# Kernel optimization log

Measured on AMD Instinct MI355X. Metric: run time of the kernel, lower is better.

Reference implementation:

```python
import jax, jax.numpy as jnp
import numpy as np

B, HH, WW, DV, DC = 4, 128, 128, 768, 128
INNER = 2 * DV          # inner_ratio * values_dim = 1536
NH = 8                  # num_heads
DH = INNER // NH        # 192
SPACING = 4
COORDS_WEIGHT = 1.0     # attention_coords_weight
EPS = 1e-6


def _anchor_idx(h, w, s, shifted=False):
    rows = np.arange(0, h, s)
    cols = np.arange(0, w, s)
    if not shifted:
        rows = rows + ((h - 1) % s) // 2
        cols = cols + ((w - 1) % s) // 2
    return rows, cols


def _rms(x, w):
    return x * jax.lax.rsqrt(jnp.mean(x * x, axis=-1, keepdims=True) + EPS) * w


def _heads(x):  # (b, n, h*d) -> (b, h, n, d)
    b, n, _ = x.shape
    return x.reshape(b, n, NH, DH).transpose(0, 2, 1, 3)


def setup_inputs() -> dict:
    key = jax.random.key(0)
    ks = jax.random.split(key, 12)
    inp = {
        "values0": jax.random.normal(ks[0], (B, HH, WW, DV), jnp.float32),
        "coords0": jax.random.normal(ks[1], (B, HH, WW, DC), jnp.float32),
        "values1": jax.random.normal(ks[2], (B, HH, WW, DV), jnp.float32),
        "coords1": jax.random.normal(ks[3], (B, HH, WW, DC), jnp.float32),
        # values_to_qkv: Linear(DV, 3*INNER, bias=False), stored as (in, out)
        "w_qkv": jax.random.normal(ks[4], (DV, 3 * INNER), jnp.float32) * (DV ** -0.5),
        "qnorm_w": jnp.ones((INNER,), jnp.float32),
        "knorm_w": jnp.ones((INNER,), jnp.float32),
        # coords_to_qk: Linear(DC, 2*INNER, bias=False) + RMSNorm(2*INNER)
        "w_coords": jax.random.normal(ks[5], (DC, 2 * INNER), jnp.float32) * (DC ** -0.5),
        "coords_norm_w": jnp.ones((2 * INNER,), jnp.float32),
        "rel_pos_weight": jax.random.normal(ks[6], (1,), jnp.float32),
        # output_proj: Linear(INNER, DV)
        "out_w": jax.random.normal(ks[7], (INNER, DV), jnp.float32) * (INNER ** -0.5),
        "out_b": jnp.zeros((DV,), jnp.float32),
    }
    return inp


def reference(values0, coords0, values1, coords1, w_qkv, qnorm_w, knorm_w,
              w_coords, coords_norm_w, rel_pos_weight, out_w, out_b):
    rows, cols = _anchor_idx(HH, WW, SPACING)
    na = len(rows) * len(cols)  # anchors per source (1024)

    def gather(x):  # (B, HH, WW, D) -> (B, na, D)
        return x[:, rows[:, None], cols].reshape(B, na, -1)

    av = jnp.concatenate([gather(values0), gather(values1)], axis=1)  # (B, 2na, DV)
    ac = jnp.concatenate([gather(coords0), gather(coords1)], axis=1)  # (B, 2na, DC)

    qv, kv, vv = jnp.split(av @ w_qkv, 3, axis=-1)
    qv = _rms(qv, qnorm_w)
    kv = _rms(kv, knorm_w)
    qc, kc = jnp.split(_rms(ac @ w_coords, coords_norm_w), 2, axis=-1)

    qv, kv, vv, qc, kc = map(_heads, (qv, kv, vv, qc, kc))  # (B, NH, N, DH)

    scale = DH ** -0.5
    dots = jnp.einsum('bhqd,bhkd->bhqk', qv, kv) * scale
    rel = jnp.einsum('bhqd,bhkd->bhqk', qc, kc) * scale
    dots = dots + (rel_pos_weight[0] * COORDS_WEIGHT) * rel
    attn = jax.nn.softmax(dots, axis=-1)

    out = jnp.einsum('bhqk,bhkd->bhqd', attn, vv)          # (B, NH, N, DH)
    out = out.transpose(0, 2, 1, 3).reshape(B, 2 * na, INNER)
    out = out @ out_w + out_b                               # (B, 2na, DV)

    a0 = out[:, :na].reshape(B, len(rows), len(cols), DV)
    a1 = out[:, na:].reshape(B, len(rows), len(cols), DV)

    o0 = values0.at[:, rows[:, None], cols, :].add(a0)
    o1 = values1.at[:, rows[:, None], cols, :].add(a1)
    return jnp.stack([o0, o1])  # (2, B, HH, WW, DV)
```

## Files before the change

### kernel.cpp

```cpp
#include <hip/hip_runtime.h>

typedef unsigned short u16;
typedef unsigned int u32;
typedef float f32x4 __attribute__((ext_vector_type(4)));
typedef short bfx8 __attribute__((ext_vector_type(8)));
typedef u16 u16x8 __attribute__((ext_vector_type(8)));
typedef u16 u16x4 __attribute__((ext_vector_type(4)));

#define MFMA_BF16(a,b,c) __builtin_amdgcn_mfma_f32_16x16x32_bf16((a),(b),(c),0,0,0)
#define GL16(src, dst) __builtin_amdgcn_global_load_lds( \
    (const __attribute__((address_space(1))) u32*)(src), \
    (__attribute__((address_space(3))) u32*)(dst), 16, 0, 0)

__device__ __forceinline__ u16 f2bf(float f) {
  unsigned u = __float_as_uint(f);
  u += 0x7fffu + ((u >> 16) & 1u);
  return (u16)(u >> 16);
}
__device__ __forceinline__ float bf2f(u16 h) {
  return __uint_as_float((unsigned)h << 16);
}

#define SCALE_ATTN 0.07216878364870323f

__global__ __launch_bounds__(256) void wtrans_kernel(
    const float* __restrict__ in, u16* __restrict__ out, int K, int N)
{
  __shared__ float tile[32][33];
  int n0 = blockIdx.x * 32, k0 = blockIdx.y * 32;
  int tx = threadIdx.x, ty = threadIdx.y;
#pragma unroll
  for (int j = 0; j < 32; j += 8)
    tile[ty + j][tx] = in[(size_t)(k0 + ty + j) * N + n0 + tx];
  __syncthreads();
#pragma unroll
  for (int j = 0; j < 32; j += 8)
    out[(size_t)(n0 + ty + j) * K + k0 + tx] = f2bf(tile[tx][ty + j]);
}

__global__ __launch_bounds__(256) void gather_kernel(
    const float* __restrict__ v0, const float* __restrict__ c0,
    const float* __restrict__ v1, const float* __restrict__ c1,
    u16* __restrict__ av, u16* __restrict__ ac)
{
  int t = blockIdx.x;
  int b = t >> 11, n = t & 2047, s = n >> 10, a = n & 1023, rr = a >> 5, cc = a & 31;
  size_t pix = ((size_t)b * 128 + (1 + 4 * rr)) * 128 + (1 + 4 * cc);
  const float4* vs = (const float4*)((s ? v1 : v0) + pix * 768);
  const float4* cs = (const float4*)((s ? c1 : c0) + pix * 128);
  int tid = threadIdx.x;
  if (tid < 192) {
    float4 f = vs[tid];
    u16x4 o = { f2bf(f.x), f2bf(f.y), f2bf(f.z), f2bf(f.w) };
    *(u16x4*)(av + (size_t)t * 768 + tid * 4) = o;
  }
  if (tid < 32) {
    float4 f = cs[tid];
    u16x4 o = { f2bf(f.x), f2bf(f.y), f2bf(f.z), f2bf(f.w) };
    *(u16x4*)(ac + (size_t)t * 128 + tid * 4) = o;
  }
}

template<int EPILOG>
__global__ __launch_bounds__(256) void gemm128(
    const u16* __restrict__ A, const u16* __restrict__ Bt,
    int K, int lda, int ldb,
    u16* __restrict__ qp, u16* __restrict__ kp, u16* __restrict__ vT,
    float* __restrict__ outAdd, const float* __restrict__ bias)
{
  __shared__ u16 As[128 * 32];
  __shared__ u16 Bs[128 * 32];
  const int tid = threadIdx.x;
  const int wid = tid >> 6, lane = tid & 63;
  const int g = lane >> 4, q15 = lane & 15;
  const int wm = wid >> 1, wn = wid & 1;
  const int m0 = blockIdx.y * 128, n0 = blockIdx.x * 128;

  const u16* ga = A + (size_t)(m0 + (tid >> 2)) * lda + (tid & 3) * 8;
  const u16* gb = Bt + (size_t)(n0 + (tid >> 2)) * ldb + (tid & 3) * 8;
  u16* lA0 = &As[tid * 8]; u16* lA1 = &As[2048 + tid * 8];
  u16* lB0 = &Bs[tid * 8]; u16* lB1 = &Bs[2048 + tid * 8];
  const size_t a64 = (size_t)64 * lda, b64 = (size_t)64 * ldb;

  const f32x4 zero = {0.f, 0.f, 0.f, 0.f};
  f32x4 acc[4][4];
#pragma unroll
  for (int i = 0; i < 4; i++)
#pragma unroll
    for (int j = 0; j < 4; j++) acc[i][j] = zero;

  for (int kk = 0; kk < K; kk += 32) {
    GL16(ga + kk, lA0);
    GL16(ga + kk + a64, lA1);
    GL16(gb + kk, lB0);
    GL16(gb + kk + b64, lB1);
    __syncthreads();
    bfx8 af[4], bf[4];
#pragma unroll
    for (int mt = 0; mt < 4; mt++)
      af[mt] = *(const bfx8*)&As[(wm * 64 + mt * 16 + q15) * 32 + g * 8];
#pragma unroll
    for (int nt = 0; nt < 4; nt++)
      bf[nt] = *(const bfx8*)&Bs[(wn * 64 + nt * 16 + q15) * 32 + g * 8];
#pragma unroll
    for (int mt = 0; mt < 4; mt++)
#pragma unroll
      for (int nt = 0; nt < 4; nt++)
        acc[mt][nt] = MFMA_BF16(af[mt], bf[nt], acc[mt][nt]);
    __syncthreads();
  }

#pragma unroll
  for (int mt = 0; mt < 4; mt++) {
#pragma unroll
    for (int nt = 0; nt < 4; nt++) {
      const int tt = m0 + wm * 64 + mt * 16 + g * 4;
      const int c = n0 + wn * 64 + nt * 16 + q15;
      f32x4 v = acc[mt][nt];
      if (EPILOG == 0) {
        int isK = c >= 1536;
        int ck = isK ? c - 1536 : c;
        int hh = ck / 192, dd = ck - hh * 192;
#pragma unroll
        for (int j = 0; j < 4; j++) {
          int t = tt + j, b = t >> 11, n = t & 2047;
          size_t ro = ((size_t)(b * 8 + hh) * 2048 + n) * 384;
          u16 val = f2bf(v[j]);
          if (!isK) qp[ro + 192 + dd] = val;
          else      kp[ro + (size_t)((((24 + (dd >> 3)) ^ (n & 7)) << 3) + (dd & 7))] = val;
        }
      } else if (EPILOG == 1) {
        float bb = bias[c];
#pragma unroll
        for (int j = 0; j < 4; j++) {
          int t = tt + j, b = t >> 11, n = t & 2047;
          int s = n >> 10, a = n & 1023, rr = a >> 5, cc2 = a & 31;
          size_t orow = (size_t)(s * 4 + b) * 16384 + (size_t)(1 + 4 * rr) * 128 + (1 + 4 * cc2);
          outAdd[orow * 768 + c] += v[j] + bb;
        }
      } else {
        if (c < 1536) {
          int hh = c / 192, dd = c - hh * 192;
#pragma unroll
          for (int j = 0; j < 4; j++) {
            int t = tt + j, b = t >> 11, n = t & 2047;
            size_t ro = ((size_t)(b * 8 + hh) * 2048 + n) * 384;
            qp[ro + dd] = f2bf(v[j]);
          }
        } else if (c < 3072) {
          int ck = c - 1536;
          int hh = ck / 192, dd = ck - hh * 192;
          int chunk = dd >> 3, e = dd & 7;
#pragma unroll
          for (int j = 0; j < 4; j++) {
            int t = tt + j, b = t >> 11, n = t & 2047;
            size_t ro = ((size_t)(b * 8 + hh) * 2048 + n) * 384;
            kp[ro + (size_t)(((chunk ^ (n & 7)) << 3) + e)] = f2bf(v[j]);
          }
        } else {
          int cv = c - 3072;
          int hh = cv / 192, dv = cv - hh * 192;
          int t0 = tt, b = t0 >> 11, n = t0 & 2047;
          u16x4 o = { f2bf(v[0]), f2bf(v[1]), f2bf(v[2]), f2bf(v[3]) };
          *(u16x4*)(vT + ((size_t)(b * 8 + hh) * 192 + dv) * 2048 + n) = o;
        }
      }
    }
  }
}

__global__ __launch_bounds__(256) void rms_all_kernel(
    u16* __restrict__ qpack, u16* __restrict__ kpack,
    const float* __restrict__ qnw, const float* __restrict__ knw,
    const float* __restrict__ cnw, const float* __restrict__ relw)
{
  __shared__ float red[3][4];
  int t = blockIdx.x, tid = threadIdx.x;
  int b = t >> 11, n = t & 2047;
  float sqv = 0.f, skv = 0.f, sc = 0.f;
  u16x8 uqv, ukv, uqc, ukc;
  size_t ro = 0;
  int c = 0;
  if (tid < 192) {
    int h = tid / 24; c = tid % 24;
    ro = ((size_t)(b * 8 + h) * 2048 + n) * 384;
    uqv = *(const u16x8*)(qpack + ro + c * 8);
    ukv = *(const u16x8*)(kpack + ro + ((c ^ (n & 7)) * 8));
    uqc = *(const u16x8*)(qpack + ro + 192 + c * 8);
    ukc = *(const u16x8*)(kpack + ro + (((24 + c) ^ (n & 7)) * 8));
#pragma unroll
    for (int e = 0; e < 8; e++) {
      float a = bf2f(uqv[e]); sqv += a * a;
      float d = bf2f(ukv[e]); skv += d * d;
      float x = bf2f(uqc[e]); sc += x * x;
      float y = bf2f(ukc[e]); sc += y * y;
    }
  }
#pragma unroll
  for (int o = 32; o >= 1; o >>= 1) {
    sqv += __shfl_xor(sqv, o); skv += __shfl_xor(skv, o); sc += __shfl_xor(sc, o);
  }
  int wv = tid >> 6;
  if ((tid & 63) == 0) { red[0][wv] = sqv; red[1][wv] = skv; red[2][wv] = sc; }
  __syncthreads();
  sqv = red[0][0] + red[0][1] + red[0][2] + red[0][3];
  skv = red[1][0] + red[1][1] + red[1][2] + red[1][3];
  sc  = red[2][0] + red[2][1] + red[2][2] + red[2][3];
  float fqv = rsqrtf(sqv * (1.f / 1536.f) + 1e-6f) * SCALE_ATTN;
  float fkv = rsqrtf(skv * (1.f / 1536.f) + 1e-6f);
  float fc  = rsqrtf(sc * (1.f / 3072.f) + 1e-6f);
  float fqc = fc * SCALE_ATTN * relw[0];
  if (tid < 192) {
    u16x8 o0, o1, o2, o3;
#pragma unroll
    for (int e = 0; e < 8; e++) {
      int col = tid * 8 + e;
      o0[e] = f2bf(bf2f(uqv[e]) * fqv * qnw[col]);
      o1[e] = f2bf(bf2f(ukv[e]) * fkv * knw[col]);
      o2[e] = f2bf(bf2f(uqc[e]) * fqc * cnw[col]);
      o3[e] = f2bf(bf2f(ukc[e]) * fc  * cnw[1536 + col]);
    }
    *(u16x8*)(qpack + ro + c * 8) = o0;
    *(u16x8*)(kpack + ro + ((c ^ (n & 7)) * 8)) = o1;
    *(u16x8*)(qpack + ro + 192 + c * 8) = o2;
    *(u16x8*)(kpack + ro + (((24 + c) ^ (n & 7)) * 8)) = o3;
  }
}

__global__ __launch_bounds__(256, 2) void attn_kernel(
    const u16* __restrict__ qpack, const u16* __restrict__ kpack,
    const u16* __restrict__ vT, u16* __restrict__ attnO)
{
  __shared__ u16 Ks[2][32 * 384];
  __shared__ u16 Vs[2][192 * 32];

  const int tid = threadIdx.x;
  const int wid = tid >> 6, lane = tid & 63;
  const int g = lane >> 4, q15 = lane & 15;
  const int bid = blockIdx.x;
  const int bh = (bid & 7) * 4 + ((bid >> 3) >> 4);
  const int q0 = ((bid >> 3) & 15) * 128 + wid * 32;
  const int b = bh >> 3, h = bh & 7;
  const int sw = q15 & 7;
  const int vsw = g ^ (q15 & 3);
  const bool hi = g >= 2;
  const int srcA = q15 + ((g & 1) << 5);

  bfx8 qf[2][12];
  {
    const u16* qb = qpack + ((size_t)bh * 2048 + q0 + q15) * 384 + g * 8;
#pragma unroll
    for (int s = 0; s < 2; s++)
#pragma unroll
      for (int c = 0; c < 12; c++)
        qf[s][c] = *(const bfx8*)(qb + s * 16 * 384 + c * 32);
  }

  const f32x4 zero = {0.f, 0.f, 0.f, 0.f};
  f32x4 acc[2][12];
#pragma unroll
  for (int s = 0; s < 2; s++)
#pragma unroll
    for (int i = 0; i < 12; i++) acc[s][i] = zero;
  float m0 = -3e30f, m1 = -3e30f, l0 = 0.f, l1 = 0.f;

  const char* kg = (const char*)(kpack + (size_t)bh * 2048 * 384);
  const char* vg = (const char*)(vT + (size_t)bh * 192 * 2048);

  auto stage = [&](int buf, int kb) {
    const char* ks = kg + (size_t)kb * 768;
#pragma unroll
    for (int j = 0; j < 6; j++) {
      int off = j * 4096 + tid * 16;
      GL16(ks + off, (char*)&Ks[buf][0] + off);
    }
    const char* vsrc = vg + (size_t)kb * 2;
#pragma unroll
    for (int j = 0; j < 3; j++) {
      int off = j * 4096 + tid * 16;
      int row = off >> 6;
      int cc = (tid & 3) ^ (row & 3);
      GL16(vsrc + (size_t)row * 4096 + cc * 16, (char*)&Vs[buf][0] + off);
    }
  };

  stage(0, 0);
  __syncthreads();

  int cur = 0;
  for (int t = 0; t < 64; t++) {
    if (t < 63) stage(cur ^ 1, (t + 1) * 32);

    f32x4 s00 = zero, s01 = zero, s10 = zero, s11 = zero;
    const u16* Kc = &Ks[cur][0];
#pragma unroll
    for (int c = 0; c < 12; c++) {
      int ch = ((((c << 2) + g) ^ sw) << 3);
      bfx8 k0 = *(const bfx8*)(Kc + q15 * 384 + ch);
      bfx8 k1 = *(const bfx8*)(Kc + (q15 + 16) * 384 + ch);
      s00 = MFMA_BF16(k0, qf[0][c], s00);
      s01 = MFMA_BF16(k0, qf[1][c], s01);
      s10 = MFMA_BF16(k1, qf[0][c], s10);
      s11 = MFMA_BF16(k1, qf[1][c], s11);
    }

    float bm0 = fmaxf(fmaxf(fmaxf(s00[0], s00[1]), fmaxf(s00[2], s00[3])),
                      fmaxf(fmaxf(s10[0], s10[1]), fmaxf(s10[2], s10[3])));
    float bm1 = fmaxf(fmaxf(fmaxf(s01[0], s01[1]), fmaxf(s01[2], s01[3])),
                      fmaxf(fmaxf(s11[0], s11[1]), fmaxf(s11[2], s11[3])));
    bm0 = fmaxf(bm0, __shfl_xor(bm0, 16)); bm0 = fmaxf(bm0, __shfl_xor(bm0, 32));
    bm1 = fmaxf(bm1, __shfl_xor(bm1, 16)); bm1 = fmaxf(bm1, __shfl_xor(bm1, 32));

    if (__any((bm0 > m0 + 8.f) | (bm1 > m1 + 8.f))) {
      float n0 = fmaxf(m0, bm0), n1 = fmaxf(m1, bm1);
      float c0 = __expf(m0 - n0), c1 = __expf(m1 - n1);
      l0 *= c0; l1 *= c1;
#pragma unroll
      for (int i = 0; i < 12; i++) {
#pragma unroll
        for (int j = 0; j < 4; j++) { acc[0][i][j] *= c0; acc[1][i][j] *= c1; }
      }
      m0 = n0; m1 = n1;
    }

    float p0[8], p1[8];
    float rs0 = 0.f, rs1 = 0.f;
#pragma unroll
    for (int j = 0; j < 4; j++) {
      p0[j]     = __expf(s00[j] - m0);
      p0[4 + j] = __expf(s10[j] - m0);
      p1[j]     = __expf(s01[j] - m1);
      p1[4 + j] = __expf(s11[j] - m1);
      rs0 += p0[j] + p0[4 + j];
      rs1 += p1[j] + p1[4 + j];
    }
    rs0 += __shfl_xor(rs0, 16); rs0 += __shfl_xor(rs0, 32);
    rs1 += __shfl_xor(rs1, 16); rs1 += __shfl_xor(rs1, 32);
    l0 += rs0; l1 += rs1;

    union { bfx8 v; u32 w[4]; } pt0, pt1;
    {
      u32 w0 = (u32)f2bf(p0[0]) | ((u32)f2bf(p0[1]) << 16);
      u32 w1 = (u32)f2bf(p0[2]) | ((u32)f2bf(p0[3]) << 16);
      u32 w2 = (u32)f2bf(p0[4]) | ((u32)f2bf(p0[5]) << 16);
      u32 w3 = (u32)f2bf(p0[6]) | ((u32)f2bf(p0[7]) << 16);
      u32 a0 = __shfl((int)w0, srcA),      b0 = __shfl((int)w2, srcA);
      u32 a1 = __shfl((int)w1, srcA),      b1 = __shfl((int)w3, srcA);
      u32 a2 = __shfl((int)w0, srcA + 16), b2 = __shfl((int)w2, srcA + 16);
      u32 a3 = __shfl((int)w1, srcA + 16), b3 = __shfl((int)w3, srcA + 16);
      pt0.w[0] = hi ? b0 : a0; pt0.w[1] = hi ? b1 : a1;
      pt0.w[2] = hi ? b2 : a2; pt0.w[3] = hi ? b3 : a3;
    }
    {
      u32 w0 = (u32)f2bf(p1[0]) | ((u32)f2bf(p1[1]) << 16);
      u32 w1 = (u32)f2bf(p1[2]) | ((u32)f2bf(p1[3]) << 16);
      u32 w2 = (u32)f2bf(p1[4]) | ((u32)f2bf(p1[5]) << 16);
      u32 w3 = (u32)f2bf(p1[6]) | ((u32)f2bf(p1[7]) << 16);
      u32 a0 = __shfl((int)w0, srcA),      b0 = __shfl((int)w2, srcA);
      u32 a1 = __shfl((int)w1, srcA),      b1 = __shfl((int)w3, srcA);
      u32 a2 = __shfl((int)w0, srcA + 16), b2 = __shfl((int)w2, srcA + 16);
      u32 a3 = __shfl((int)w1, srcA + 16), b3 = __shfl((int)w3, srcA + 16);
      pt1.w[0] = hi ? b0 : a0; pt1.w[1] = hi ? b1 : a1;
      pt1.w[2] = hi ? b2 : a2; pt1.w[3] = hi ? b3 : a3;
    }

    const u16* Vc = &Vs[cur][0];
#pragma unroll
    for (int dt = 0; dt < 12; dt++) {
      bfx8 vf = *(const bfx8*)(Vc + dt * 512 + q15 * 32 + vsw * 8);
      acc[0][dt] = MFMA_BF16(vf, pt0.v, acc[0][dt]);
      acc[1][dt] = MFMA_BF16(vf, pt1.v, acc[1][dt]);
    }

    asm volatile("s_waitcnt vmcnt(0)" ::: "memory");
    __syncthreads();
    cur ^= 1;
  }

  float li0 = 1.f / l0, li1 = 1.f / l1;
  u16* ob = attnO + ((size_t)(b * 2048 + q0 + q15)) * 1536 + h * 192;
#pragma unroll
  for (int dt = 0; dt < 12; dt++) {
    u16x4 o0, o1;
#pragma unroll
    for (int j = 0; j < 4; j++) {
      o0[j] = f2bf(acc[0][dt][j] * li0);
      o1[j] = f2bf(acc[1][dt][j] * li1);
    }
    *(u16x4*)(ob + dt * 16 + g * 4) = o0;
    *(u16x4*)(ob + (size_t)16 * 1536 + dt * 16 + g * 4) = o1;
  }
}

extern "C" void kernel_launch(void* const* d_in, const int* in_sizes, int n_in,
                              void* d_out, int out_size, void* d_ws, size_t ws_size,
                              hipStream_t stream)
{
  const float* values0 = (const float*)d_in[0];
  const float* coords0 = (const float*)d_in[1];
  const float* values1 = (const float*)d_in[2];
  const float* coords1 = (const float*)d_in[3];
  const float* w_qkv   = (const float*)d_in[4];
  const float* qnorm_w = (const float*)d_in[5];
  const float* knorm_w = (const float*)d_in[6];
  const float* w_coords= (const float*)d_in[7];
  const float* cnorm_w = (const float*)d_in[8];
  const float* relw    = (const float*)d_in[9];
  const float* out_w   = (const float*)d_in[10];
  const float* out_b   = (const float*)d_in[11];
  float* out = (float*)d_out;
  (void)in_sizes; (void)n_in; (void)out_size; (void)ws_size;

  char* ws = (char*)d_ws;
  u16* qpack   = (u16*)(ws);
  u16* kpack   = (u16*)(ws + 50331648ull);
  u16* vT      = (u16*)(ws + 100663296ull);
  u16* attnO   = (u16*)(ws + 125829120ull);
  u16* av      = (u16*)(ws + 150994944ull);
  u16* ac      = (u16*)(ws + 163577856ull);
  u16* wqkvT   = (u16*)(ws + 165675008ull);
  u16* wcoordT = (u16*)(ws + 172752896ull);
  u16* outwT   = (u16*)(ws + 173539328ull);

  const size_t HALF = 50331648ull;
  hipMemcpyAsync(out, values0, HALF * 4, hipMemcpyDeviceToDevice, stream);
  hipMemcpyAsync(out + HALF, values1, HALF * 4, hipMemcpyDeviceToDevice, stream);

  wtrans_kernel<<<dim3(144, 24), dim3(32, 8), 0, stream>>>(w_qkv, wqkvT, 768, 4608);
  wtrans_kernel<<<dim3(96, 4),   dim3(32, 8), 0, stream>>>(w_coords, wcoordT, 128, 3072);
  wtrans_kernel<<<dim3(24, 48),  dim3(32, 8), 0, stream>>>(out_w, outwT, 1536, 768);
  gather_kernel<<<8192, 256, 0, stream>>>(values0, coords0, values1, coords1, av, ac);

  gemm128<2><<<dim3(36, 64), 256, 0, stream>>>(av, wqkvT, 768, 768, 768,
                                               qpack, kpack, vT, nullptr, nullptr);
  gemm128<0><<<dim3(24, 64), 256, 0, stream>>>(ac, wcoordT, 128, 128, 128,
                                               qpack, kpack, nullptr, nullptr, nullptr);

  rms_all_kernel<<<8192, 256, 0, stream>>>(qpack, kpack, qnorm_w, knorm_w, cnorm_w, relw);

  attn_kernel<<<512, 256, 0, stream>>>(qpack, kpack, vT, attnO);

  gemm128<1><<<dim3(6, 64), 256, 0, stream>>>(attnO, outwT, 1536, 1536, 1536,
                                              nullptr, nullptr, nullptr, out, out_b);
}
```

Baseline: 562.0 us.

## Fuse output base copy into attention kernel and defer softmax row reductions

Drops the two device-to-device copies of values0/values1 into the output. Instead, each attention block copies a strided slab of float4s on every key-tile iteration, so the bandwidth-bound copy overlaps with the MFMA-bound attention loop. The MFMA sections are also wrapped in s_setprio. The cross-lane shuffles for the row max and row sum are moved off the per-iteration path: the max reduction now runs only when a rescale is triggered, and the sum is reduced once after the loop. The risk is that the extra global traffic and register pressure slow the attention loop and only partly hide the copy cost.

```diff
diff --git a/kernel.cpp b/kernel.cpp
--- a/kernel.cpp
+++ b/kernel.cpp
@@ -229,7 +229,9 @@
 
 __global__ __launch_bounds__(256, 2) void attn_kernel(
     const u16* __restrict__ qpack, const u16* __restrict__ kpack,
-    const u16* __restrict__ vT, u16* __restrict__ attnO)
+    const u16* __restrict__ vT, u16* __restrict__ attnO,
+    const float* __restrict__ cpy_v0, const float* __restrict__ cpy_v1,
+    float* __restrict__ cpy_out)
 {
   __shared__ u16 Ks[2][32 * 384];
   __shared__ u16 Vs[2][192 * 32];
@@ -246,6 +248,13 @@
   const bool hi = g >= 2;
   const int srcA = q15 + ((g & 1) << 5);
 
+  const float4* cs0 = (const float4*)cpy_v0;
+  const float4* cs1 = (const float4*)cpy_v1;
+  float4* cdst = (float4*)cpy_out;
+  const size_t cgid = (size_t)bid * 256 + tid;
+  const size_t CHALF = 12582912ull;
+  const size_t CSLAB = 8388608ull;
+
   bfx8 qf[2][12];
   {
     const u16* qb = qpack + ((size_t)bh * 2048 + q0 + q15) * 384 + g * 8;
@@ -291,8 +300,20 @@
   for (int t = 0; t < 64; t++) {
     if (t < 63) stage(cur ^ 1, (t + 1) * 32);
 
+    const size_t cbase = (size_t)t * 131072ull + cgid;
+    float4 cr0, cr1, cr2;
+    {
+      size_t i0 = cbase;
+      size_t i1 = cbase + CSLAB;
+      size_t i2 = cbase + 2 * CSLAB;
+      cr0 = (i0 < CHALF) ? cs0[i0] : cs1[i0 - CHALF];
+      cr1 = (i1 < CHALF) ? cs0[i1] : cs1[i1 - CHALF];
+      cr2 = (i2 < CHALF) ? cs0[i2] : cs1[i2 - CHALF];
+    }
+
     f32x4 s00 = zero, s01 = zero, s10 = zero, s11 = zero;
     const u16* Kc = &Ks[cur][0];
+    __builtin_amdgcn_s_setprio(1);
 #pragma unroll
     for (int c = 0; c < 12; c++) {
       int ch = ((((c << 2) + g) ^ sw) << 3);
@@ -303,15 +324,16 @@
       s10 = MFMA_BF16(k1, qf[0][c], s10);
       s11 = MFMA_BF16(k1, qf[1][c], s11);
     }
+    __builtin_amdgcn_s_setprio(0);
 
     float bm0 = fmaxf(fmaxf(fmaxf(s00[0], s00[1]), fmaxf(s00[2], s00[3])),
                       fmaxf(fmaxf(s10[0], s10[1]), fmaxf(s10[2], s10[3])));
     float bm1 = fmaxf(fmaxf(fmaxf(s01[0], s01[1]), fmaxf(s01[2], s01[3])),
                       fmaxf(fmaxf(s11[0], s11[1]), fmaxf(s11[2], s11[3])));
-    bm0 = fmaxf(bm0, __shfl_xor(bm0, 16)); bm0 = fmaxf(bm0, __shfl_xor(bm0, 32));
-    bm1 = fmaxf(bm1, __shfl_xor(bm1, 16)); bm1 = fmaxf(bm1, __shfl_xor(bm1, 32));
 
     if (__any((bm0 > m0 + 8.f) | (bm1 > m1 + 8.f))) {
+      bm0 = fmaxf(bm0, __shfl_xor(bm0, 16)); bm0 = fmaxf(bm0, __shfl_xor(bm0, 32));
+      bm1 = fmaxf(bm1, __shfl_xor(bm1, 16)); bm1 = fmaxf(bm1, __shfl_xor(bm1, 32));
       float n0 = fmaxf(m0, bm0), n1 = fmaxf(m1, bm1);
       float c0 = __expf(m0 - n0), c1 = __expf(m1 - n1);
       l0 *= c0; l1 *= c1;
@@ -334,8 +356,6 @@
       rs0 += p0[j] + p0[4 + j];
       rs1 += p1[j] + p1[4 + j];
     }
-    rs0 += __shfl_xor(rs0, 16); rs0 += __shfl_xor(rs0, 32);
-    rs1 += __shfl_xor(rs1, 16); rs1 += __shfl_xor(rs1, 32);
     l0 += rs0; l1 += rs1;
 
     union { bfx8 v; u32 w[4]; } pt0, pt1;
@@ -365,17 +385,29 @@
     }
 
     const u16* Vc = &Vs[cur][0];
+    __builtin_amdgcn_s_setprio(1);
 #pragma unroll
     for (int dt = 0; dt < 12; dt++) {
       bfx8 vf = *(const bfx8*)(Vc + dt * 512 + q15 * 32 + vsw * 8);
       acc[0][dt] = MFMA_BF16(vf, pt0.v, acc[0][dt]);
       acc[1][dt] = MFMA_BF16(vf, pt1.v, acc[1][dt]);
     }
+    __builtin_amdgcn_s_setprio(0);
+
+    {
+      size_t i0 = cbase;
+      size_t i1 = cbase + CSLAB;
+      size_t i2 = cbase + 2 * CSLAB;
+      cdst[i0] = cr0; cdst[i1] = cr1; cdst[i2] = cr2;
+    }
 
     asm volatile("s_waitcnt vmcnt(0)" ::: "memory");
     __syncthreads();
     cur ^= 1;
   }
+
+  l0 += __shfl_xor(l0, 16); l0 += __shfl_xor(l0, 32);
+  l1 += __shfl_xor(l1, 16); l1 += __shfl_xor(l1, 32);
 
   float li0 = 1.f / l0, li1 = 1.f / l1;
   u16* ob = attnO + ((size_t)(b * 2048 + q0 + q15)) * 1536 + h * 192;
@@ -422,10 +454,6 @@
   u16* wcoordT = (u16*)(ws + 172752896ull);
   u16* outwT   = (u16*)(ws + 173539328ull);
 
-  const size_t HALF = 50331648ull;
-  hipMemcpyAsync(out, values0, HALF * 4, hipMemcpyDeviceToDevice, stream);
-  hipMemcpyAsync(out + HALF, values1, HALF * 4, hipMemcpyDeviceToDevice, stream);
-
   wtrans_kernel<<<dim3(144, 24), dim3(32, 8), 0, stream>>>(w_qkv, wqkvT, 768, 4608);
   wtrans_kernel<<<dim3(96, 4),   dim3(32, 8), 0, stream>>>(w_coords, wcoordT, 128, 3072);
   wtrans_kernel<<<dim3(24, 48),  dim3(32, 8), 0, stream>>>(out_w, outwT, 1536, 768);
@@ -438,7 +466,8 @@
 
   rms_all_kernel<<<8192, 256, 0, stream>>>(qpack, kpack, qnorm_w, knorm_w, cnorm_w, relw);
 
-  attn_kernel<<<512, 256, 0, stream>>>(qpack, kpack, vT, attnO);
+  attn_kernel<<<512, 256, 0, stream>>>(qpack, kpack, vT, attnO,
+                                       values0, values1, out);
 
   gemm128<1><<<dim3(6, 64), 256, 0, stream>>>(attnO, outwT, 1536, 1536, 1536,
                                               nullptr, nullptr, nullptr, out, out_b);
```

Measured after the change: 581.8 us. 1.04x slower.
